# Kernel tuning notes

Hardware: AMD Instinct MI355X
Metric: run time of the kernel (lower is better)

## Reference

```python
import jax, jax.numpy as jnp
import numpy as np

NUM_BITS = 2
QN = -(2 ** (NUM_BITS - 1))          # -2 (signed)
QP = 2 ** (NUM_BITS - 1) - 1         # 1
NUM_LEVELS = 2 ** NUM_BITS           # 4


def setup_inputs() -> dict:
    key = jax.random.key(0)
    k1, k2 = jax.random.split(key)
    # Large transformer FFN weight matrix: d_model=4096, d_ff=16384
    weights = jax.random.normal(k1, (4096, 16384), dtype=jnp.float32) * 0.1
    alpha = jax.random.uniform(k2, (1,), dtype=jnp.float32, minval=0.05, maxval=0.2)
    return {"weights": weights, "alpha": alpha}


def reference(weights, alpha):
    # backprop_to_alpha=False -> alpha is detached everywhere (torch uses .item())
    a = jax.lax.stop_gradient(alpha[0])
    w = weights.reshape(-1)

    # LSQ quantization levels: [Qn*a, ..., -a, 0, a, ..., Qp*a]
    levels = jnp.arange(QN, QP + 1, dtype=w.dtype) * a            # [NUM_LEVELS]

    # Bin assignment by LSQ integer code (non-differentiable indices)
    bins = jnp.round(jnp.clip(w / a, QN, QP)).astype(jnp.int32)   # in [QN, QP]
    idx = bins - QN                                               # in [0, NUM_LEVELS)

    # Single-pass per-bin sum / sumsq / count (replaces per-bin mask loop)
    count = jax.ops.segment_sum(jnp.ones_like(w), idx, num_segments=NUM_LEVELS)
    s = jax.ops.segment_sum(w, idx, num_segments=NUM_LEVELS)
    sq = jax.ops.segment_sum(w * w, idx, num_segments=NUM_LEVELS)

    safe = jnp.maximum(count, 1.0)
    mean = s / safe
    var = sq / safe - mean * mean                                 # biased (unbiased=False)

    total_mse = jnp.sum(jnp.where(count > 0, (mean - levels) ** 2, 0.0))
    total_var = jnp.sum(jnp.where(count >= 2, var, 0.0))
    loss = total_mse + total_var

    # Diagnostics (computed under no_grad in torch)
    wq = bins.astype(w.dtype) * a                                 # quantized weights
    d = jax.lax.stop_gradient(w - wq)
    mean_distance = jnp.mean(jnp.abs(d))
    quantization_mse = jnp.mean(d * d)

    return jnp.stack([loss, total_mse, total_var, quantization_mse, mean_distance])
```

## Files before the change

kernel.cpp:

```cpp
#include <hip/hip_runtime.h>
#include <cstdint>

#define TS 16384
#define NSLOT 13
#define NCH 7
#define NW 4096
#define FCAP 512
#define FLQ 256


__device__ __forceinline__ int kbin_th(float x, double T1, double T2) {
    double xd = (double)x;
    if (xd >   T1) return 1;
    if (xd >= -T1) return 0;
    if (xd >  -T2) return -1;
    return -2;
}

__device__ __forceinline__ double wred64(double v) {
#pragma unroll
    for (int d = 32; d >= 1; d >>= 1) v += __shfl_xor(v, d, 64);
    return v;
}
__device__ __forceinline__ int wred32i(int v) {
#pragma unroll
    for (int d = 32; d >= 1; d >>= 1) v += __shfl_xor(v, d, 64);
    return v;
}

__device__ __forceinline__ int expo_bits(double A) {
    const long long b = __double_as_longlong(A);
    return (int)((b >> 52) & 0x7FF) - 1023;
}
__device__ __forceinline__ int emin_of(double A0) {
    if (!(A0 > 0.0)) return 12345;
    const int e = expo_bits(A0);
    if (e < -100 || e > 100) return 12345;
    return e;
}

__global__ __launch_bounds__(64) void zero2(double* __restrict__ diag,
        float* __restrict__ chains, double* __restrict__ A0d) {
    if (threadIdx.x < 8) {
        diag[threadIdx.x] = 0.0;
        chains[threadIdx.x] = 0.0f;
        A0d[threadIdx.x] = 0.0;
    }
}

__global__ __launch_bounds__(256) void part1(const float* __restrict__ w,
        const float* __restrict__ alpha, int* __restrict__ hist,
        double* __restrict__ dpart, long long n, long long nsegw)
{
    const float a = alpha[0];
    const double T1 = (double)a * (0.5 + 0x1p-25);
    const double T2 = (double)a * (1.5 - 0x1p-24);
    const int wv = threadIdx.x >> 6, lane = threadIdx.x & 63;
    const int sid = blockIdx.x * 4 + wv;
    const long long seg = (long long)sid * nsegw;
    long long send = seg + nsegw; if (send > n) send = n;
    int h0=0,h1=0,h2=0,h3=0;
    double ad=0.0, dd=0.0, s0=0.0;

    for (long long base = seg; base < send; base += 256) {
        const long long i = base + (long long)lane * 4;
        if (i >= send) break;
        float4 v;
        if (i + 3 < send) v = *reinterpret_cast<const float4*>(w + i);
        else {
            v = make_float4(0.f,0.f,0.f,0.f);
            v.x = w[i];
            if (i+1 < send) v.y = w[i+1];
            if (i+2 < send) v.z = w[i+2];
        }
        const float xs[4] = {v.x, v.y, v.z, v.w};
        const int nv = (int)((send - i) < 4 ? (send - i) : 4);
#pragma unroll
        for (int j = 0; j < 4; ++j) {
            if (j >= nv) break;
            const float x = xs[j];
            const int k = kbin_th(x, T1, T2);
            h0 += (k==-2); h1 += (k==-1); h2 += (k==0); h3 += (k==1);
            const float bf = (float)k;
            const float wq = __fmul_rn(bf, a);
            const float d  = __fsub_rn(x, wq);
            ad += (double)fabsf(d);
            dd += (double)__fmul_rn(d, d);
            if (k == 0) s0 += (double)x;
        }
    }

    h0 = wred32i(h0); h1 = wred32i(h1); h2 = wred32i(h2); h3 = wred32i(h3);
    ad = wred64(ad);  dd = wred64(dd);  s0 = wred64(s0);

    if (lane == 0) {
        hist[sid*4 + 0] = h0;
        hist[sid*4 + 1] = h1;
        hist[sid*4 + 2] = h2;
        hist[sid*4 + 3] = h3;
        dpart[sid*4 + 0] = ad;
        dpart[sid*4 + 1] = dd;
        dpart[sid*4 + 2] = s0;
    }
}

__global__ __launch_bounds__(256) void scank(const int* __restrict__ hist,
        const double* __restrict__ dpart, int* __restrict__ bbase,
        int* __restrict__ hdr, double* __restrict__ diag)
{
    const int wv = threadIdx.x >> 6, lane = threadIdx.x & 63;
    if (wv < 4) {
        int running = 0;
        for (int c = 0; c < NW/64; ++c) {
            int v = hist[(c*64 + lane)*4 + wv];
            int p = v;
#pragma unroll
            for (int d = 1; d < 64; d <<= 1) {
                int t = __shfl_up(p, d, 64);
                if (lane >= d) p += t;
            }
            bbase[(c*64+lane)*4 + wv] = running + p - v;
            running += __shfl(p, 63, 64);
        }
        if (lane == 0) hdr[wv] = running;
    }
    __syncthreads();
    if (threadIdx.x == 0) {
        int b = 0;
        for (int q = 0; q < 4; ++q) { hdr[4+q] = b; b += (hdr[q] + 63) & ~63; }
    }

    double a0=0.0, a1=0.0, a2=0.0;
    for (int e = threadIdx.x; e < NW; e += 256) {
        a0 += dpart[e*4+0]; a1 += dpart[e*4+1]; a2 += dpart[e*4+2];
    }
    a0 = wred64(a0); a1 = wred64(a1); a2 = wred64(a2);
    __shared__ double dsh[4][3];
    if (lane == 0) { dsh[wv][0]=a0; dsh[wv][1]=a1; dsh[wv][2]=a2; }
    __syncthreads();
    if (threadIdx.x == 0) {
        diag[0] = dsh[0][0]+dsh[1][0]+dsh[2][0]+dsh[3][0];
        diag[1] = dsh[0][1]+dsh[1][1]+dsh[2][1]+dsh[3][1];
        diag[2] = dsh[0][2]+dsh[1][2]+dsh[2][2]+dsh[3][2];
    }
}

__global__ __launch_bounds__(256) void part2(const float* __restrict__ w,
        const float* __restrict__ alpha, const int* __restrict__ bbase,
        const int* __restrict__ hdr, float* __restrict__ streams,
        long long n, long long nsegw)
{
    const float a = alpha[0];
    const double T1 = (double)a * (0.5 + 0x1p-25);
    const double T2 = (double)a * (1.5 - 0x1p-24);
    __shared__ float buf[4][4][FCAP + 8];
    const int wv = threadIdx.x >> 6, lane = threadIdx.x & 63;
    const int sid = blockIdx.x * 4 + wv;
    const unsigned long long ltmask = (1ULL << lane) - 1ULL;

    int run[4], fill[4];
#pragma unroll
    for (int b = 0; b < 4; ++b) {
        run[b]  = hdr[4+b] + bbase[sid*4 + b];
        fill[b] = 0;
    }

    const long long seg = (long long)sid * nsegw;
    long long send = seg + nsegw; if (send > n) send = n;

    for (long long base = seg; base < send; base += 256) {
#pragma unroll
        for (int j = 0; j < 4; ++j) {
            const long long idx = base + j*64 + lane;
            float x = 0.f; int k = 9;
            if (idx < send) { x = w[idx]; k = kbin_th(x, T1, T2); }
#pragma unroll
            for (int b = 0; b < 4; ++b) {
                const unsigned long long bal = __ballot(k == b - 2);
                if (k == b - 2) {
                    const int rank = __popcll(bal & ltmask);
                    buf[wv][b][fill[b] + rank] = x;
                }
                fill[b] += __popcll(bal);
            }
        }
#pragma unroll
        for (int b = 0; b < 4; ++b) {
            if (fill[b] >= FLQ) {
#pragma unroll
                for (int r = 0; r < FLQ/64; ++r)
                    streams[(long long)run[b] + r*64 + lane] = buf[wv][b][r*64 + lane];
                const int rem = fill[b] - FLQ;
                float tmp[4];
#pragma unroll
                for (int r = 0; r < 4; ++r) {
                    const int ir = lane + r*64;
                    tmp[r] = (ir < rem) ? buf[wv][b][FLQ + ir] : 0.f;
                }
#pragma unroll
                for (int r = 0; r < 4; ++r) {
                    const int ir = lane + r*64;
                    if (ir < rem) buf[wv][b][ir] = tmp[r];
                }
                run[b] += FLQ; fill[b] = rem;
            }
        }
    }
#pragma unroll
    for (int b = 0; b < 4; ++b) {
        for (int i2 = lane; i2 < fill[b]; i2 += 64)
            streams[(long long)run[b] + i2] = buf[wv][b][i2];
    }
}

__device__ void span_st(const float* __restrict__ p, int isq,
                        double& A, long long lo, long long hi, int lane)
{
    for (long long base = lo; base < hi; base += 4096) {
        float xs[64];
        const long long e0 = base + (long long)lane * 64;
#pragma unroll
        for (int q4 = 0; q4 < 16; ++q4) {
            const long long fi = e0 + q4 * 4;
            float4 v = make_float4(0.f,0.f,0.f,0.f);
            if (fi + 3 < hi) v = *reinterpret_cast<const float4*>(p + fi);
            else {
                if (fi     < hi) v.x = p[fi];
                if (fi + 1 < hi) v.y = p[fi + 1];
                if (fi + 2 < hi) v.z = p[fi + 2];
            }
            xs[q4*4+0]=v.x; xs[q4*4+1]=v.y; xs[q4*4+2]=v.z; xs[q4*4+3]=v.w;
        }
#pragma unroll
        for (int j = 0; j < 64; ++j) {
            const float x = xs[j];
            xs[j] = isq ? __fmul_rn(x, x) : fabsf(x);
        }

        int C = 0;
        while (C < 64) {
            if (A > 0.0) {
                const int e = ilogb(A);
                const double u  = ldexp(1.0, e - 23);
                const double Bb = ldexp(1.0, e + 1);
                const double sc = ldexp(1.0, 23 - e);
                double kd = 0.0;
                if (lane >= C) {
#pragma unroll
                    for (int j = 0; j < 64; ++j) kd += rint((double)xs[j] * sc);
                }
                const bool big = kd >= 1099511627776.0;
                double pp = kd;
#pragma unroll
                for (int d = 1; d < 64; d <<= 1) {
                    double tt = __shfl_up(pp, d, 64);
                    if (lane >= d) pp += tt;
                }
                const bool cross = (lane >= C) && (big || (A + u * pp >= Bb));
                const unsigned long long bal = __ballot(cross);
                if (bal == 0ULL) {
                    A = A + u * __shfl(pp, 63);
                    break;
                }
                const int F = __ffsll((long long)bal) - 1;
                double An = 0.0;
                if (lane == F) {
                    const double Aex = A + u * (pp - kd);
                    float Af = (float)Aex;
#pragma unroll
                    for (int j = 0; j < 64; ++j) Af = __fadd_rn(Af, xs[j]);
                    An = (double)Af;
                }
                A = __shfl(An, F);
                C = F + 1;
            } else {
                bool has = false;
                if (lane >= C) {
#pragma unroll
                    for (int j = 0; j < 64; ++j) has = has || (xs[j] > 0.0f);
                }
                const unsigned long long bal = __ballot(has);
                if (bal == 0ULL) break;
                const int F = __ffsll((long long)bal) - 1;
                double An = 0.0;
                if (lane == F) {
                    float Af = 0.0f;
#pragma unroll
                    for (int j = 0; j < 64; ++j) Af = __fadd_rn(Af, xs[j]);
                    An = (double)Af;
                }
                A = __shfl(An, F);
                C = F + 1;
            }
        }
    }
}

__global__ __launch_bounds__(64) void span0(const float* __restrict__ streams,
        const int* __restrict__ hdr, double* __restrict__ A0d)
{
    const int ch = blockIdx.x;
    const int STR[NCH] = {0,1,3,0,1,2,3};
    const int ISQ[NCH] = {0,0,0,1,1,1,1};
    const int st = STR[ch];
    const long long cnt = (long long)hdr[st];
    const float* p = streams + hdr[4+st];
    double A = 0.0;
    if (cnt > 0)
        span_st(p, ISQ[ch], A, 0LL, (TS < cnt ? (long long)TS : cnt), threadIdx.x);
    if (threadIdx.x == 0) A0d[ch] = A;
}

template<int HASS>
__device__ __forceinline__ void passA_two(const float* __restrict__ p,
        long long cnt, double* __restrict__ krowS, double* __restrict__ krowQ,
        float baseS, float baseQ, long long ntg, long long tile)
{
    const long long lo = tile * TS;
    long long hi = lo + TS; if (hi > cnt) hi = cnt;

    float scS[NSLOT], scQ[NSLOT];
    scS[0] = baseS; scQ[0] = baseQ;
#pragma unroll
    for (int s = 1; s < NSLOT; ++s) { scS[s] = scS[s-1]*0.5f; scQ[s] = scQ[s-1]*0.5f; }
    int accS[NSLOT], accQ[NSLOT];
#pragma unroll
    for (int s = 0; s < NSLOT; ++s) { accS[s] = 0; accQ[s] = 0; }

    const int tid = threadIdx.x;
    for (long long i = lo + (long long)tid*4; i < hi; i += 256*4) {
        float4 v;
        if (i + 3 < hi) v = *reinterpret_cast<const float4*>(p + i);
        else {
            v = make_float4(0.f,0.f,0.f,0.f);
            v.x = p[i];
            if (i+1 < hi) v.y = p[i+1];
            if (i+2 < hi) v.z = p[i+2];
        }
        const float xsv[4] = {v.x, v.y, v.z, v.w};
#pragma unroll
        for (int j = 0; j < 4; ++j) {
            const float x  = xsv[j];
            const float xq = __fmul_rn(x, x);
            if (HASS) {
                const float ax = fabsf(x);
#pragma unroll
                for (int s = 0; s < NSLOT; ++s)
                    accS[s] += (int)rintf(ax * scS[s]);
            }
#pragma unroll
            for (int s = 0; s < NSLOT; ++s)
                accQ[s] += (int)rintf(xq * scQ[s]);
        }
    }

    __shared__ double lred[4][2*NSLOT];
    const int lane = tid & 63, wv = tid >> 6;
#pragma unroll
    for (int s = 0; s < NSLOT; ++s) {
        double rs = wred64((double)accS[s]);
        double rq = wred64((double)accQ[s]);
        if (lane == 0) { lred[wv][s] = rs; lred[wv][NSLOT+s] = rq; }
    }
    __syncthreads();
    if (tid < 2*NSLOT) {
        const double sum = lred[0][tid]+lred[1][tid]+lred[2][tid]+lred[3][tid];
        if (tid < NSLOT) {
            if (HASS) krowS[(long long)tid * ntg + tile] = sum;
        } else {
            krowQ[(long long)(tid-NSLOT) * ntg + tile] = sum;
        }
    }
}

__global__ __launch_bounds__(256) void passA7(const float* __restrict__ streams,
        const int* __restrict__ hdr, const double* __restrict__ A0d,
        double* __restrict__ Ktab, long long ntg)
{
    const int st = blockIdx.y;
    const int SCH[4] = {0, 1, -1, 2};
    const int QCH[4] = {3, 4,  5, 6};
    const long long cnt = (long long)hdr[st];
    const long long tile = blockIdx.x;
    if (tile * TS >= cnt) return;
    const float* p = streams + hdr[4+st];

    const int qch = QCH[st];
    const int emQ = emin_of(A0d[qch]);
    const float baseQ = (emQ == 12345) ? 0.0f : ldexpf(1.0f, 23 - emQ);
    double* krowQ = Ktab + (long long)qch * NSLOT * ntg;

    if (SCH[st] >= 0) {
        const int sch = SCH[st];
        const int emS = emin_of(A0d[sch]);
        const float baseS = (emS == 12345) ? 0.0f : ldexpf(1.0f, 23 - emS);
        double* krowS = Ktab + (long long)sch * NSLOT * ntg;
        passA_two<1>(p, cnt, krowS, krowQ, baseS, baseQ, ntg, tile);
    } else {
        passA_two<0>(p, cnt, nullptr, krowQ, 0.0f, baseQ, ntg, tile);
    }
}

__global__ __launch_bounds__(64) void walk2(const float* __restrict__ streams,
        const int* __restrict__ hdr, const double* __restrict__ A0d,
        const double* __restrict__ Ktab, float* __restrict__ chains, long long ntg)
{
    const int ch = blockIdx.x;
    const int lane = threadIdx.x;
    const int STR[NCH]  = {0,1,3,0,1,2,3};
    const int ISQ[NCH]  = {0,0,0,1,1,1,1};
    const int OSLOT[NCH]= {0,1,3,4,5,6,7};
    const int st = STR[ch], isq = ISQ[ch];
    const long long cnt = (long long)hdr[st];
    const float* p = streams + hdr[4+st];
    const long long ntiles = (cnt + TS - 1) / TS;
    const double* krow = Ktab + (long long)ch * NSLOT * ntg;
    const int em = emin_of(A0d[ch]);

    double A = A0d[ch];
    long long t = 1;
    while (t < ntiles) {
        if (A > 0.0 && em != 12345) {
            const int e = expo_bits(A);
            const int slot = e - em;
            if (slot >= 0 && slot < NSLOT) {
                const long long wt = t + lane;
                double Kv = (wt < ntiles) ? krow[(long long)slot * ntg + wt] : 0.0;
                double P = Kv;
#pragma unroll
                for (int d = 1; d < 64; d <<= 1) {
                    double tt = __shfl_up(P, d, 64);
                    if (lane >= d) P += tt;
                }
                const double u  = ldexp(1.0, e - 23);
                const double Bb = ldexp(1.0, e + 1);
                const bool bad = (A + u * P > Bb);
                const unsigned long long bal = __ballot(bad);
                if (bal == 0ULL) { A += u * __shfl(P, 63); t += 64; continue; }
                const int F = __ffsll((long long)bal) - 1;
                if (F > 0) { A += u * __shfl(P, F - 1); t += F; }
                const long long lo = t * (long long)TS;
                long long hi = lo + TS; if (hi > cnt) hi = cnt;
                span_st(p, isq, A, lo, hi, lane);
                ++t;
                continue;
            }
        }
        const long long lo = t * (long long)TS;
        long long hi = lo + TS; if (hi > cnt) hi = cnt;
        span_st(p, isq, A, lo, hi, lane);
        ++t;
    }
    if (lane == 0) chains[OSLOT[ch]] = (float)A;
}

__global__ void fin2(const float* __restrict__ chains,
                     const double* __restrict__ diag,
                     const int* __restrict__ hdr,
                     const float* __restrict__ alpha,
                     float* __restrict__ out, long long n)
{
    const float a = alpha[0];
    const float s_np[4]  = { -chains[0], -chains[1], (float)diag[2], chains[3] };
    const float sq_np[4] = {  chains[4],  chains[5],  chains[6],     chains[7] };
    float tmse = 0.f, tvar = 0.f;
#pragma unroll
    for (int b = 0; b < 4; ++b) {
        float cnt = fminf((float)hdr[b], 16777216.0f);
        float safe = fmaxf(cnt, 1.0f);
        float mean = __fdiv_rn(s_np[b], safe);
        float var  = __fsub_rn(__fdiv_rn(sq_np[b], safe), __fmul_rn(mean, mean));
        float lvl  = __fmul_rn((float)(b - 2), a);
        float e    = __fsub_rn(mean, lvl);
        if (cnt > 0.f)  tmse = __fadd_rn(tmse, __fmul_rn(e, e));
        if (cnt >= 2.f) tvar = __fadd_rn(tvar, var);
    }
    out[0] = __fadd_rn(tmse, tvar);
    out[1] = tmse;
    out[2] = tvar;
    out[3] = (float)(diag[1] / (double)n);
    out[4] = (float)(diag[0] / (double)n);
}

__global__ __launch_bounds__(64) void zero_diag6(double* __restrict__ diag) {
    if (threadIdx.x < 6) diag[threadIdx.x] = 0.0;
}
__global__ __launch_bounds__(256) void diag6(const float* __restrict__ w,
        const float* __restrict__ alpha, double* __restrict__ diag, int n4, long long n)
{
    const float a = alpha[0];
    float ad = 0.f, dd = 0.f; int c0=0,c1=0,c2=0,c3=0;
    auto pe = [&](float x) {
        float r = __fdiv_rn(x, a);
        float cl = fminf(1.0f, fmaxf(-2.0f, r));
        float bf = rintf(cl); int k = (int)bf;
        float wq = __fmul_rn(bf, a); float d = __fsub_rn(x, wq);
        ad = __fadd_rn(ad, fabsf(d)); dd = __fadd_rn(dd, __fmul_rn(d, d));
        if (k==-2) c0++; else if (k==-1) c1++; else if (k==0) c2++; else c3++;
    };
    const float4* w4 = reinterpret_cast<const float4*>(w);
    const int stride = gridDim.x * 256;
    for (int i = blockIdx.x * 256 + threadIdx.x; i < n4; i += stride) {
        float4 v = w4[i]; pe(v.x); pe(v.y); pe(v.z); pe(v.w);
    }
    if (blockIdx.x == 0 && threadIdx.x == 0)
        for (long long i = (long long)n4 * 4; i < n; ++i) pe(w[i]);
    double vals[6] = {(double)ad,(double)dd,(double)c0,(double)c1,(double)c2,(double)c3};
    __shared__ double red[256];
    const int tid = threadIdx.x;
#pragma unroll
    for (int j = 0; j < 6; ++j) {
        red[tid] = vals[j]; __syncthreads();
        for (int s = 128; s > 0; s >>= 1) { if (tid < s) red[tid] += red[tid+s]; __syncthreads(); }
        if (tid == 0) atomicAdd(&diag[j], red[0]);
        __syncthreads();
    }
}
__global__ __launch_bounds__(64) void seq_chains(const float* __restrict__ w,
        const float* __restrict__ alpha, float* __restrict__ chains, long long n)
{
    const float a = alpha[0];
    const int lane = threadIdx.x; const int myrow = lane & 7;
    __shared__ float val[8][64];
    float acc = 0.0f;
    const long long ntl = (n + 63) / 64;
    float x_next = (lane < n) ? w[lane] : 0.0f;
    for (long long t = 0; t < ntl; ++t) {
        float x = x_next;
        { long long idxn = (t + 1) * 64 + lane; x_next = (idxn < n) ? w[idxn] : 0.0f; }
        const long long idx = t * 64 + lane;
        const bool valid = (idx < n);
        float r = __fdiv_rn(x, a);
        float cl = fminf(1.0f, fmaxf(-2.0f, r));
        int k = (int)rintf(cl); int row = k + 2;
        float xx = __fmul_rn(x, x);
#pragma unroll
        for (int b = 0; b < 4; ++b) {
            val[b][lane]     = (valid && row == b) ? x  : 0.0f;
            val[4 + b][lane] = (valid && row == b) ? xx : 0.0f;
        }
        __syncthreads();
        if (lane < 8) {
#pragma unroll
            for (int e4i = 0; e4i < 16; ++e4i) {
                float4 v = *reinterpret_cast<const float4*>(&val[myrow][e4i * 4]);
                acc = __fadd_rn(acc, v.x); acc = __fadd_rn(acc, v.y);
                acc = __fadd_rn(acc, v.z); acc = __fadd_rn(acc, v.w);
            }
        }
        __syncthreads();
    }
    if (lane < 8) chains[lane] = acc;
}
__global__ void fin_seq(const float* __restrict__ chains, const double* __restrict__ diag,
                        const float* __restrict__ alpha, float* __restrict__ out, long long n)
{
    const float a = alpha[0];
    float tmse = 0.0f, tvar = 0.0f;
#pragma unroll
    for (int b = 0; b < 4; ++b) {
        float cnt = fminf((float)diag[2 + b], 16777216.0f);
        float safe = fmaxf(cnt, 1.0f);
        float mean = __fdiv_rn(chains[b], safe);
        float var  = __fsub_rn(__fdiv_rn(chains[4 + b], safe), __fmul_rn(mean, mean));
        float lvl  = __fmul_rn((float)(b - 2), a);
        float e    = __fsub_rn(mean, lvl);
        if (cnt > 0.0f)  tmse = __fadd_rn(tmse, __fmul_rn(e, e));
        if (cnt >= 2.0f) tvar = __fadd_rn(tvar, var);
    }
    out[0] = __fadd_rn(tmse, tvar);
    out[1] = tmse; out[2] = tvar;
    out[3] = (float)(diag[1] / (double)n);
    out[4] = (float)(diag[0] / (double)n);
}

extern "C" void kernel_launch(void* const* d_in, const int* in_sizes, int n_in,
                              void* d_out, int out_size, void* d_ws, size_t ws_size,
                              hipStream_t stream) {
    const float* w     = (const float*)d_in[0];
    const float* alpha = (const float*)d_in[1];
    float* out = (float*)d_out;
    const long long n = (long long)in_sizes[0];
    const long long ntg = (n + TS - 1) / TS;

    size_t off = 0;
    const size_t ktab_off = off;   off += (size_t)NCH * NSLOT * ntg * 8;
    const size_t hist_off = off;   off += (size_t)NW * 4 * 4;
    const size_t bbase_off = off;  off += (size_t)NW * 4 * 4;
    const size_t hdr_off = off;    off += 8 * 4;
    const size_t diag_off = (off + 7) & ~(size_t)7;  off = diag_off + 8 * 8;
    const size_t dpart_off = off;  off += (size_t)NW * 4 * 8;
    const size_t a0_off = off;     off += 8 * 8;
    const size_t chains_off = off; off += 8 * 4;
    const size_t streams_off = (off + 255) & ~(size_t)255;
    const size_t need1 = streams_off + ((size_t)n + 512) * 4;

    if (ws_size >= need1) {
        double* Ktab   = (double*)((char*)d_ws + ktab_off);
        int*    hist   = (int*)   ((char*)d_ws + hist_off);
        int*    bbase  = (int*)   ((char*)d_ws + bbase_off);
        int*    hdr    = (int*)   ((char*)d_ws + hdr_off);
        double* diag   = (double*)((char*)d_ws + diag_off);
        double* dpart  = (double*)((char*)d_ws + dpart_off);
        double* A0d    = (double*)((char*)d_ws + a0_off);
        float*  chains = (float*) ((char*)d_ws + chains_off);
        float*  strm   = (float*) ((char*)d_ws + streams_off);
        long long nsegw = ((n + NW - 1) / NW + 255) & ~255LL;

        zero2<<<1, 64, 0, stream>>>(diag, chains, A0d);
        part1<<<NW/4, 256, 0, stream>>>(w, alpha, hist, dpart, n, nsegw);
        scank<<<1, 256, 0, stream>>>(hist, dpart, bbase, hdr, diag);
        part2<<<NW/4, 256, 0, stream>>>(w, alpha, bbase, hdr, strm, n, nsegw);
        span0<<<NCH, 64, 0, stream>>>(strm, hdr, A0d);
        dim3 ga((unsigned)ntg, 4);
        passA7<<<ga, 256, 0, stream>>>(strm, hdr, A0d, Ktab, ntg);
        walk2<<<NCH, 64, 0, stream>>>(strm, hdr, A0d, Ktab, chains, ntg);
        fin2<<<1, 1, 0, stream>>>(chains, diag, hdr, alpha, out, n);
    } else {
        float*  chains = (float*)d_ws;
        double* diag   = (double*)((char*)d_ws + 128);
        zero_diag6<<<1, 64, 0, stream>>>(diag);
        diag6<<<1024, 256, 0, stream>>>(w, alpha, diag, (int)(n >> 2), n);
        seq_chains<<<1, 64, 0, stream>>>(w, alpha, chains, n);
        fin_seq<<<1, 1, 0, stream>>>(chains, diag, alpha, out, n);
    }
}
```

Baseline: 641.7 us.

## Scatter binned weights directly to global streams without LDS staging buffer

The partition kernel now loads four contiguous floats per lane with a float4 and computes per-bin ranks with ballots over all four elements. It writes each element straight to its global stream slot instead of staging in a shared-memory FIFO and flushing in 256-element chunks. This removes LDS traffic, the flush and compaction logic, and the shared buffer, which can raise occupancy. The cost is that global stores become scattered across four streams per wave, so they coalesce less well than the previous chunked flushes. Element order inside a stream changes but stays deterministic.

```diff
diff --git a/kernel.cpp b/kernel.cpp
--- a/kernel.cpp
+++ b/kernel.cpp
@@ -5,8 +5,6 @@
 #define NSLOT 13
 #define NCH 7
 #define NW 4096
-#define FCAP 512
-#define FLQ 256
 
 
 __device__ __forceinline__ int kbin_th(float x, double T1, double T2) {
@@ -153,63 +151,59 @@
     const float a = alpha[0];
     const double T1 = (double)a * (0.5 + 0x1p-25);
     const double T2 = (double)a * (1.5 - 0x1p-24);
-    __shared__ float buf[4][4][FCAP + 8];
     const int wv = threadIdx.x >> 6, lane = threadIdx.x & 63;
     const int sid = blockIdx.x * 4 + wv;
     const unsigned long long ltmask = (1ULL << lane) - 1ULL;
 
-    int run[4], fill[4];
-#pragma unroll
-    for (int b = 0; b < 4; ++b) {
-        run[b]  = hdr[4+b] + bbase[sid*4 + b];
-        fill[b] = 0;
-    }
+    int run0 = hdr[4+0] + bbase[sid*4 + 0];
+    int run1 = hdr[4+1] + bbase[sid*4 + 1];
+    int run2 = hdr[4+2] + bbase[sid*4 + 2];
+    int run3 = hdr[4+3] + bbase[sid*4 + 3];
 
     const long long seg = (long long)sid * nsegw;
     long long send = seg + nsegw; if (send > n) send = n;
 
     for (long long base = seg; base < send; base += 256) {
+        const long long i = base + (long long)lane * 4;
+        float xs[4]; int kk[4];
+        if (i + 3 < send) {
+            const float4 v = *reinterpret_cast<const float4*>(w + i);
+            xs[0]=v.x; xs[1]=v.y; xs[2]=v.z; xs[3]=v.w;
+            kk[0]=kbin_th(xs[0],T1,T2); kk[1]=kbin_th(xs[1],T1,T2);
+            kk[2]=kbin_th(xs[2],T1,T2); kk[3]=kbin_th(xs[3],T1,T2);
+        } else {
+#pragma unroll
+            for (int j = 0; j < 4; ++j) {
+                const long long idx = i + j;
+                if (idx < send) { xs[j] = w[idx]; kk[j] = kbin_th(xs[j],T1,T2); }
+                else            { xs[j] = 0.f;   kk[j] = 9; }
+            }
+        }
+
+        int br0=0,br1=0,br2=0,br3=0;
+        int tt0=0,tt1=0,tt2=0,tt3=0;
 #pragma unroll
         for (int j = 0; j < 4; ++j) {
-            const long long idx = base + j*64 + lane;
-            float x = 0.f; int k = 9;
-            if (idx < send) { x = w[idx]; k = kbin_th(x, T1, T2); }
-#pragma unroll
-            for (int b = 0; b < 4; ++b) {
-                const unsigned long long bal = __ballot(k == b - 2);
-                if (k == b - 2) {
-                    const int rank = __popcll(bal & ltmask);
-                    buf[wv][b][fill[b] + rank] = x;
-                }
-                fill[b] += __popcll(bal);
-            }
-        }
-#pragma unroll
-        for (int b = 0; b < 4; ++b) {
-            if (fill[b] >= FLQ) {
-#pragma unroll
-                for (int r = 0; r < FLQ/64; ++r)
-                    streams[(long long)run[b] + r*64 + lane] = buf[wv][b][r*64 + lane];
-                const int rem = fill[b] - FLQ;
-                float tmp[4];
-#pragma unroll
-                for (int r = 0; r < 4; ++r) {
-                    const int ir = lane + r*64;
-                    tmp[r] = (ir < rem) ? buf[wv][b][FLQ + ir] : 0.f;
-                }
-#pragma unroll
-                for (int r = 0; r < 4; ++r) {
-                    const int ir = lane + r*64;
-                    if (ir < rem) buf[wv][b][ir] = tmp[r];
-                }
-                run[b] += FLQ; fill[b] = rem;
-            }
-        }
-    }
-#pragma unroll
-    for (int b = 0; b < 4; ++b) {
-        for (int i2 = lane; i2 < fill[b]; i2 += 64)
-            streams[(long long)run[b] + i2] = buf[wv][b][i2];
+            const unsigned long long b0 = __ballot(kk[j] == -2);
+            const unsigned long long b1 = __ballot(kk[j] == -1);
+            const unsigned long long b2 = __ballot(kk[j] ==  0);
+            const unsigned long long b3 = __ballot(kk[j] ==  1);
+            br0 += __popcll(b0 & ltmask); tt0 += __popcll(b0);
+            br1 += __popcll(b1 & ltmask); tt1 += __popcll(b1);
+            br2 += __popcll(b2 & ltmask); tt2 += __popcll(b2);
+            br3 += __popcll(b3 & ltmask); tt3 += __popcll(b3);
+        }
+
+        int own0=0, own1=0, own2=0, own3=0;
+#pragma unroll
+        for (int j = 0; j < 4; ++j) {
+            const int k = kk[j];
+            if      (k == -2) { streams[(long long)(run0 + br0 + own0)] = xs[j]; ++own0; }
+            else if (k == -1) { streams[(long long)(run1 + br1 + own1)] = xs[j]; ++own1; }
+            else if (k ==  0) { streams[(long long)(run2 + br2 + own2)] = xs[j]; ++own2; }
+            else if (k ==  1) { streams[(long long)(run3 + br3 + own3)] = xs[j]; ++own3; }
+        }
+        run0 += tt0; run1 += tt1; run2 += tt2; run3 += tt3;
     }
 }
 
```

New measurement: 575.5 us. 10.3% less time.
